# Kernel optimization log

Measured on AMD Instinct MI355X. Metric: run time of the kernel, lower is better.

## Reference

```python
import jax, jax.numpy as jnp
import numpy as np

M = 262144
GRID_SIZE = 1024
L1_BITS = 15            # 3 * log2(1024/32): top bits of morton give the 32^3 L1 cell
L1_CELLS = 32 * 32 * 32
MAX_EXT = 4             # 4^3 = 64 == oversized_threshold_voxels
OVERSIZED_THRESHOLD = 64
VOXEL_SIZE_FACTOR = 3.0
CLIP_Q = 0.01
PAD = 0.1
CHI2_95_3 = 7.814727903251179  # chi2.ppf(0.95, df=3)
SENTINEL = np.int64(1 << 30)   # larger than any 30-bit morton code
EPS = 1e-7


def quat_to_rotmat(q):
    q = q / (jnp.linalg.norm(q, axis=-1, keepdims=True) + EPS)
    w, x, y, z = q[..., 0], q[..., 1], q[..., 2], q[..., 3]
    R = jnp.stack([
        1 - 2 * (y * y + z * z), 2 * (x * y - w * z), 2 * (x * z + w * y),
        2 * (x * y + w * z), 1 - 2 * (x * x + z * z), 2 * (y * z - w * x),
        2 * (x * z - w * y), 2 * (y * z + w * x), 1 - 2 * (x * x + y * y),
    ], axis=-1)
    return R.reshape(q.shape[:-1] + (3, 3))


def expand_bits_10(v):
    x = v.astype(jnp.uint32)
    x = (x | (x << 16)) & jnp.uint32(0x030000FF)
    x = (x | (x << 8)) & jnp.uint32(0x0300F00F)
    x = (x | (x << 4)) & jnp.uint32(0x030C30C3)
    x = (x | (x << 2)) & jnp.uint32(0x09249249)
    return x


def encode_morton(c):
    # c: [..., 3] int32 grid coords -> uint32 morton
    ci = jnp.clip(c, 0, 1023).astype(jnp.uint32)
    return (expand_bits_10(ci[..., 0]) << 2) | (expand_bits_10(ci[..., 1]) << 1) | expand_bits_10(ci[..., 2])


def setup_inputs() -> dict:
    key = jax.random.key(0)
    k1, k2, k3 = jax.random.split(key, 3)
    positions = jax.random.normal(k1, (M, 3), dtype=jnp.float32) * 10.0
    scales = jax.random.uniform(k2, (M, 3), dtype=jnp.float32) * 0.02 + 0.002
    quats = jax.random.normal(k3, (M, 4), dtype=jnp.float32)
    return {"positions": positions, "scales": scales, "quats": quats}


def reference(positions, scales, quats):
    m = positions.shape[0]
    # 1) per-sphere AABB from confidence ellipsoid of Sigma = R diag(s^2) R^T
    R = quat_to_rotmat(quats)
    k = jnp.sqrt(jnp.float32(CHI2_95_3))
    radius = k * jnp.sqrt(jnp.einsum('mij,mj->mi', R * R, scales * scales) + 1e-12)  # [M,3]
    min_corners = positions - radius
    max_corners = positions + radius
    # robust global AABB: quantile clip + padding
    gmin = jnp.quantile(min_corners, CLIP_Q, axis=0)
    gmax = jnp.quantile(max_corners, 1.0 - CLIP_Q, axis=0)
    extent = gmax - gmin
    global_min = gmin - PAD * extent
    voxel_size = jnp.median(radius[:, 0]) * VOXEL_SIZE_FACTOR
    # 2) enumerate sphere-voxel pairs (fixed 4x4x4 window per sphere, masked)
    g_min = jnp.clip(jnp.floor((min_corners - global_min) / voxel_size).astype(jnp.int32), 0, GRID_SIZE - 1)
    g_max = jnp.clip(jnp.floor((max_corners - global_min) / voxel_size).astype(jnp.int32), 0, GRID_SIZE - 1)
    ext = g_max - g_min + 1                       # [M,3]
    nvox = ext[:, 0] * ext[:, 1] * ext[:, 2]
    oversized = (nvox > OVERSIZED_THRESHOLD) | jnp.any(ext > MAX_EXT, axis=-1)
    d = jnp.arange(MAX_EXT, dtype=jnp.int32)
    offs = jnp.stack(jnp.meshgrid(d, d, d, indexing='ij'), axis=-1).reshape(-1, 3)  # [64,3]
    coords = g_min[:, None, :] + offs[None, :, :]  # [M,64,3]
    valid = jnp.all(offs[None] < ext[:, None, :], axis=-1) & (~oversized[:, None])  # [M,64]
    morton = encode_morton(coords).astype(jnp.int64)  # [M,64]
    morton = jnp.where(valid, morton, SENTINEL)
    sphere_id = jnp.where(valid, jnp.arange(m, dtype=jnp.int32)[:, None], jnp.int32(-1))
    mf = morton.reshape(-1)
    sf = sphere_id.reshape(-1)
    # 3) sort pairs by morton code (invalid/sentinel entries compact to the end)
    order = jnp.argsort(mf)
    sm = mf[order]
    ss = sf[order]
    total_pairs = jnp.sum(valid).astype(jnp.int32)
    # 4) L1 lookup table: start offset of each 32^3 coarse cell in sorted pairs
    l1keys = sm >> L1_BITS
    cells = jnp.arange(L1_CELLS, dtype=sm.dtype)
    left = jnp.searchsorted(l1keys, cells, side='left')
    right = jnp.searchsorted(l1keys, cells, side='right')
    l1_offsets = jnp.where(right > left, left, -1).astype(jnp.int32)
    # unique occupied voxels
    valid_s = sm < SENTINEL
    is_new = jnp.concatenate([valid_s[:1], valid_s[1:] & (sm[1:] != sm[:-1])])
    num_unique = jnp.sum(is_new).astype(jnp.int32)
    # 5) precompute sphere data: Sigma^{-1} = R diag(s^-2) R^T, Gaussian norm factor
    inv_s2 = 1.0 / (scales * scales + 1e-12)
    cov_inv = jnp.einsum('mij,mj,mkj->mik', R, inv_s2, R)
    norm_factor = 1.0 / (((2.0 * jnp.pi) ** 1.5) * jnp.prod(scales, axis=-1) + EPS)
    return (sm, ss, oversized.astype(jnp.int32), l1_offsets, total_pairs, num_unique,
            global_min.astype(jnp.float32), voxel_size.astype(jnp.float32), cov_inv, norm_factor)
```

## Files before the change

### kernel.cpp

```cpp
#include <hip/hip_runtime.h>
#include <stdint.h>
#include <math.h>

#define MS 262144
#define NPAIR 16777216
#define RBINS 1024
#define SORT_TILE 2048
#define MAXC (4u*1048576u)
#define OUTK_BLOCKS 2048

#define OFF_SELHIST   0u
#define OFF_SELSTATE  114688u
#define OFF_SELVALS   114800u
#define OFF_DEVN      114856u
#define OFF_DEVU      114860u
#define OFF_SCANPART  114864u
#define OFF_SCANBASE  115888u
#define OFF_PARAMS    116912u
#define WS_ZERO_BYTES 131072u
#define OFF_CORNERS   ((size_t)131072)
#define OFF_GMP       (OFF_CORNERS + (size_t)7*MS*4)
#define OFF_EXTP      (OFF_GMP + (size_t)MS*4)
#define OFF_COUNTS    (OFF_EXTP + (size_t)MS*4)
#define OFF_OFFS      (OFF_COUNTS + (size_t)MS*4)
#define FIXED_WS      (OFF_OFFS + (size_t)MS*4)

#define O_SM   0u
#define O_SS   16777216u
#define O_OV   33554432u
#define O_L1   33816576u
#define O_TP   33849344u
#define O_NU   33849345u
#define O_GMIN 33849346u
#define O_VOX  33849349u
#define O_COV  33849350u
#define O_NF   36208646u

__constant__ uint32_t RANKS[14] = {2621u,2622u,2621u,2622u,2621u,2622u,
                                   259521u,259522u,259521u,259522u,259521u,259522u,
                                   131071u,131072u};

__device__ __forceinline__ uint32_t fkey(float f) {
  uint32_t u = __float_as_uint(f);
  return (u & 0x80000000u) ? ~u : (u | 0x80000000u);
}
__device__ __forceinline__ float unfkey(uint32_t u) {
  uint32_t b = (u & 0x80000000u) ? (u ^ 0x80000000u) : ~u;
  return __uint_as_float(b);
}
__device__ __forceinline__ uint32_t expand10(uint32_t x) {
  x = (x | (x << 16)) & 0x030000FFu;
  x = (x | (x << 8))  & 0x0300F00Fu;
  x = (x | (x << 4))  & 0x030C30C3u;
  x = (x | (x << 2))  & 0x09249249u;
  return x;
}

__global__ void sphere_kernel(const float* __restrict__ pos,
                              const float* __restrict__ scl,
                              const float* __restrict__ qt,
                              float* __restrict__ corners,
                              float* __restrict__ out) {
#pragma clang fp contract(off)
  int i = blockIdx.x * 256 + threadIdx.x;
  if (i >= MS) return;
  float qw = qt[4*i+0], qx = qt[4*i+1], qy = qt[4*i+2], qz = qt[4*i+3];
  float ssum = (((qw*qw) + (qx*qx)) + (qy*qy)) + (qz*qz);
  float nrm = sqrtf(ssum);
  float den = nrm + 1e-7f;
  float w = qw / den, x = qx / den, y = qy / den, z = qz / den;
  float xx=x*x, yy=y*y, zz=z*z, xy=x*y, xz=x*z, yz=y*z, wx=w*x, wy=w*y, wz=w*z;
  float R00 = 1.0f - 2.0f*(yy+zz);
  float R01 = 2.0f*(xy-wz);
  float R02 = 2.0f*(xz+wy);
  float R10 = 2.0f*(xy+wz);
  float R11 = 1.0f - 2.0f*(xx+zz);
  float R12 = 2.0f*(yz-wx);
  float R20 = 2.0f*(xz-wy);
  float R21 = 2.0f*(yz+wx);
  float R22 = 1.0f - 2.0f*(xx+yy);
  float s0 = scl[3*i+0], s1 = scl[3*i+1], s2c = scl[3*i+2];
  float t0 = s0*s0, t1 = s1*s1, t2 = s2c*s2c;
  const float KC = sqrtf(7.814727903251179f);
  float d0 = (((R00*R00)*t0) + ((R01*R01)*t1)) + ((R02*R02)*t2);
  float d1 = (((R10*R10)*t0) + ((R11*R11)*t1)) + ((R12*R12)*t2);
  float d2 = (((R20*R20)*t0) + ((R21*R21)*t1)) + ((R22*R22)*t2);
  float r0 = KC * sqrtf(d0 + 1e-12f);
  float r1 = KC * sqrtf(d1 + 1e-12f);
  float r2 = KC * sqrtf(d2 + 1e-12f);
  float px = pos[3*i+0], py = pos[3*i+1], pz = pos[3*i+2];
  corners[(size_t)0*MS+i] = px - r0;
  corners[(size_t)1*MS+i] = py - r1;
  corners[(size_t)2*MS+i] = pz - r2;
  corners[(size_t)3*MS+i] = px + r0;
  corners[(size_t)4*MS+i] = py + r1;
  corners[(size_t)5*MS+i] = pz + r2;
  corners[(size_t)6*MS+i] = r0;
  float i0 = 1.0f / (t0 + 1e-12f);
  float i1 = 1.0f / (t1 + 1e-12f);
  float i2 = 1.0f / (t2 + 1e-12f);
  float* cv = out + O_COV + (size_t)i*9;
  cv[0] = ((R00*i0)*R00 + (R01*i1)*R01) + (R02*i2)*R02;
  cv[1] = ((R00*i0)*R10 + (R01*i1)*R11) + (R02*i2)*R12;
  cv[2] = ((R00*i0)*R20 + (R01*i1)*R21) + (R02*i2)*R22;
  cv[3] = ((R10*i0)*R00 + (R11*i1)*R01) + (R12*i2)*R02;
  cv[4] = ((R10*i0)*R10 + (R11*i1)*R11) + (R12*i2)*R12;
  cv[5] = ((R10*i0)*R20 + (R11*i1)*R21) + (R12*i2)*R22;
  cv[6] = ((R20*i0)*R00 + (R21*i1)*R01) + (R22*i2)*R02;
  cv[7] = ((R20*i0)*R10 + (R21*i1)*R11) + (R22*i2)*R12;
  cv[8] = ((R20*i0)*R20 + (R21*i1)*R21) + (R22*i2)*R22;
  out[O_NF + i] = 1.0f / ((15.749609945722419f * ((s0*s1)*s2c)) + 1e-7f);
}

__global__ void sel_hist(const float* __restrict__ corners,
                         const uint32_t* __restrict__ selstate,
                         uint32_t* __restrict__ selhist, int round) {
  __shared__ uint32_t h[2048];
  int j = blockIdx.y;
  const float* a = corners + (size_t)(j >> 1) * MS;
  for (int d = threadIdx.x; d < 2048; d += 256) h[d] = 0;
  __syncthreads();
  uint32_t pref = 0;
  int dshift = 21, pshift = 31, maskb = 2047;
  if (round == 1) { pref = selstate[2*j]; dshift = 10; pshift = 21; }
  else if (round == 2) { pref = selstate[2*j]; dshift = 0; pshift = 10; maskb = 1023; }
  int base = blockIdx.x * 4096;
  for (int t = threadIdx.x; t < 4096; t += 256) {
    uint32_t u = fkey(a[base + t]);
    bool ok = (round == 0) || ((u >> pshift) == pref);
    if (ok) atomicAdd(&h[(u >> dshift) & (uint32_t)maskb], 1u);
  }
  __syncthreads();
  uint32_t* gh = selhist + (size_t)j * 2048;
  for (int d = threadIdx.x; d < 2048; d += 256) {
    uint32_t c = h[d];
    if (c) atomicAdd(&gh[d], c);
  }
}

__global__ void sel_fin(uint32_t* __restrict__ selhist,
                        uint32_t* __restrict__ selstate,
                        uint32_t* __restrict__ selvals, int round) {
  __shared__ uint32_t part[256];
  int j = blockIdx.x;
  uint32_t* h = selhist + (size_t)j * 2048;
  int bins = (round == 2) ? 1024 : 2048;
  uint32_t s = 0;
  int gbase = threadIdx.x * 8;
  #pragma unroll
  for (int b = 0; b < 8; b++) { int d = gbase + b; s += (d < bins) ? h[d] : 0u; }
  part[threadIdx.x] = s;
  __syncthreads();
  if (threadIdx.x == 0) {
    uint32_t rank = (round == 0) ? RANKS[j] : selstate[2*j+1];
    uint32_t run = 0; int grp = 0;
    for (; grp < 255; grp++) { uint32_t p = part[grp]; if (rank < run + p) break; run += p; }
    uint32_t dig = 0;
    for (int b = 0; b < 8; b++) {
      int d = grp*8 + b; uint32_t c = (d < bins) ? h[d] : 0u;
      if (rank < run + c) { dig = (uint32_t)d; break; }
      run += c;
    }
    rank -= run;
    uint32_t pref;
    if (round == 0) pref = dig;
    else if (round == 1) pref = (selstate[2*j] << 11) | dig;
    else pref = (selstate[2*j] << 10) | dig;
    selstate[2*j] = pref; selstate[2*j+1] = rank;
    if (round == 2) selvals[j] = pref;
  }
  __syncthreads();
  for (int d = threadIdx.x; d < 2048; d += 256) h[d] = 0;
}

__global__ void params_kernel(const uint32_t* __restrict__ selvals,
                              float* __restrict__ params, float* __restrict__ out) {
#pragma clang fp contract(off)
  if (threadIdx.x != 0 || blockIdx.x != 0) return;
  float v[14];
  for (int j = 0; j < 14; j++) v[j] = unfkey(selvals[j]);
  float g1   = (float)(0.01 * 262143.0 - 2621.0);
  float t2   = (float)(0.99 * 262143.0 - 259521.0);
  float omt2 = 1.0f - t2;
  float gmin[3], gmax[3];
  for (int a = 0; a < 3; a++) {
    float lo = v[2*a], hi = v[2*a+1];
    float d  = hi - lo;
    gmin[a] = lo + d * g1;
  }
  for (int a = 0; a < 3; a++) {
    float lo = v[6+2*a], hi = v[7+2*a];
    float d  = hi - lo;
    gmax[a] = hi - d * omt2;
  }
  float med = (v[12] + v[13]) * 0.5f;
  float vox = med * 3.0f;
  for (int a = 0; a < 3; a++) {
    float ext = gmax[a] - gmin[a];
    float gm  = gmin[a] - 0.1f * ext;
    params[a] = gm;
    out[O_GMIN + a] = gm;
  }
  params[3] = vox;
  out[O_VOX] = vox;
}

__global__ void grid_kernel(const float* __restrict__ corners,
                            const float* __restrict__ params,
                            uint32_t* __restrict__ gmp, uint32_t* __restrict__ extp,
                            uint32_t* __restrict__ counts, float* __restrict__ out) {
#pragma clang fp contract(off)
  int i = blockIdx.x * 256 + threadIdx.x;
  if (i >= MS) return;
  float vox = params[3];
  int g0[3], g1[3];
  for (int a = 0; a < 3; a++) {
    float gm = params[a];
    float lo = corners[(size_t)a*MS + i];
    float hi = corners[(size_t)(a+3)*MS + i];
    int lq = (int)floorf((lo - gm) / vox);
    int hq = (int)floorf((hi - gm) / vox);
    g0[a] = min(max(lq, 0), 1023);
    g1[a] = min(max(hq, 0), 1023);
  }
  int ex = g1[0]-g0[0]+1, ey = g1[1]-g0[1]+1, ez = g1[2]-g0[2]+1;
  int nv = ex*ey*ez;
  bool ovs = (nv > 64) || (ex > 4) || (ey > 4) || (ez > 4);
  out[O_OV + i] = ovs ? 1.0f : 0.0f;
  gmp[i] = (uint32_t)g0[0] | ((uint32_t)g0[1] << 10) | ((uint32_t)g0[2] << 20);
  extp[i] = ovs ? 0u : ((uint32_t)ex | ((uint32_t)ey << 8) | ((uint32_t)ez << 16));
  counts[i] = ovs ? 0u : (uint32_t)nv;
}

__global__ void scan1(const uint32_t* __restrict__ counts, uint32_t* __restrict__ offs,
                      uint32_t* __restrict__ part) {
  __shared__ uint32_t sh[256];
  int b = blockIdx.x, tid = threadIdx.x;
  int base = b * 1024 + tid * 4;
  uint32_t v0 = counts[base], v1 = counts[base+1], v2 = counts[base+2], v3 = counts[base+3];
  uint32_t sum = v0+v1+v2+v3;
  sh[tid] = sum; __syncthreads();
  for (int off = 1; off < 256; off <<= 1) {
    uint32_t x = (tid >= off) ? sh[tid-off] : 0u;
    __syncthreads();
    sh[tid] += x;
    __syncthreads();
  }
  uint32_t excl = sh[tid] - sum;
  if (tid == 255) part[b] = sh[255];
  offs[base] = excl; offs[base+1] = excl+v0; offs[base+2] = excl+v0+v1; offs[base+3] = excl+v0+v1+v2;
}

__global__ void scan2(const uint32_t* __restrict__ part, uint32_t* __restrict__ sbase,
                      uint32_t* __restrict__ devN, uint32_t cap) {
  __shared__ uint32_t sh[256];
  int tid = threadIdx.x;
  uint32_t v = part[tid];
  sh[tid] = v; __syncthreads();
  for (int off = 1; off < 256; off <<= 1) {
    uint32_t x = (tid >= off) ? sh[tid-off] : 0u;
    __syncthreads();
    sh[tid] += x;
    __syncthreads();
  }
  sbase[tid] = sh[tid] - v;
  if (tid == 255) *devN = min(sh[255], cap);
}

__global__ void emit_pairs(const uint32_t* __restrict__ gmp, const uint32_t* __restrict__ extp,
                           const uint32_t* __restrict__ offs, const uint32_t* __restrict__ sbase,
                           uint32_t* __restrict__ akey, uint32_t* __restrict__ aval,
                           uint32_t cap) {
  int i = blockIdx.x * 256 + threadIdx.x;
  if (i >= MS) return;
  uint32_t ep = extp[i];
  if (!ep) return;
  uint32_t p = offs[i] + sbase[i >> 10];
  if (p >= cap) return;
  uint32_t gp = gmp[i];
  int gx = gp & 1023, gy = (gp >> 10) & 1023, gz = (gp >> 20) & 1023;
  int ex = ep & 255, ey = (ep >> 8) & 255, ez = (ep >> 16) & 255;
  for (int dx = 0; dx < ex; dx++) {
    uint32_t mx = expand10((uint32_t)(gx+dx)) << 2;
    for (int dy = 0; dy < ey; dy++) {
      uint32_t mxy = mx | (expand10((uint32_t)(gy+dy)) << 1);
      for (int dz = 0; dz < ez; dz++) {
        if (p < cap) { akey[p] = mxy | expand10((uint32_t)(gz+dz)); aval[p] = (uint32_t)i; }
        p++;
      }
    }
  }
}

__global__ void rdx_hist(const uint32_t* __restrict__ keys, const uint32_t* __restrict__ devN,
                         uint32_t* __restrict__ ctab, int shift, int nt) {
  __shared__ uint32_t h[RBINS];
  int t = blockIdx.x;
  for (int i = threadIdx.x; i < RBINS; i += 256) h[i] = 0;
  __syncthreads();
  int N = (int)*devN;
  int base = t * SORT_TILE;
  int cnt = min(SORT_TILE, N - base);
  if (cnt == SORT_TILE) {
    const uint4* k4 = reinterpret_cast<const uint4*>(keys + base);
    #pragma unroll
    for (int j = 0; j < 2; j++) {
      uint4 k = k4[j * 256 + threadIdx.x];
      atomicAdd(&h[(k.x >> shift) & (RBINS-1)], 1u);
      atomicAdd(&h[(k.y >> shift) & (RBINS-1)], 1u);
      atomicAdd(&h[(k.z >> shift) & (RBINS-1)], 1u);
      atomicAdd(&h[(k.w >> shift) & (RBINS-1)], 1u);
    }
  } else {
    for (int i = threadIdx.x; i < cnt; i += 256)
      atomicAdd(&h[(keys[base + i] >> shift) & (RBINS - 1)], 1u);
  }
  __syncthreads();
  for (int i = threadIdx.x; i < RBINS; i += 256) ctab[(size_t)i * nt + t] = h[i];
}

__global__ void rdx_colscan(uint32_t* __restrict__ ctab, uint32_t* __restrict__ dtot, int nt) {
  __shared__ uint32_t sh[256];
  int d = blockIdx.x, tid = threadIdx.x;
  uint32_t* row = ctab + (size_t)d * nt;
  int per = nt >> 8;
  uint32_t v[8];
  uint32_t s = 0;
  const uint4* r4 = reinterpret_cast<const uint4*>(row + tid * per);
  #pragma unroll
  for (int j = 0; j < 2; j++) {
    uint4 q = r4[j];
    v[j*4+0]=q.x; v[j*4+1]=q.y; v[j*4+2]=q.z; v[j*4+3]=q.w;
    s += q.x+q.y+q.z+q.w;
  }
  sh[tid] = s; __syncthreads();
  for (int off = 1; off < 256; off <<= 1) {
    uint32_t x = (tid >= off) ? sh[tid - off] : 0u;
    __syncthreads();
    sh[tid] += x;
    __syncthreads();
  }
  uint32_t excl = sh[tid] - s;
  uint4* w4 = reinterpret_cast<uint4*>(row + tid * per);
  #pragma unroll
  for (int j = 0; j < 2; j++) {
    uint4 q;
    q.x = excl; excl += v[j*4+0];
    q.y = excl; excl += v[j*4+1];
    q.z = excl; excl += v[j*4+2];
    q.w = excl; excl += v[j*4+3];
    w4[j] = q;
  }
  if (tid == 255) dtot[d] = excl;
}

__global__ void rdx_basescan(const uint32_t* __restrict__ dtot, uint32_t* __restrict__ dbase) {
  __shared__ uint32_t sh[256];
  int tid = threadIdx.x;
  uint32_t run = 0;
  for (int c = 0; c < RBINS; c += 256) {
    uint32_t v = dtot[c + tid];
    sh[tid] = v; __syncthreads();
    for (int off = 1; off < 256; off <<= 1) {
      uint32_t x = (tid >= off) ? sh[tid - off] : 0u;
      __syncthreads();
      sh[tid] += x;
      __syncthreads();
    }
    dbase[c + tid] = run + (sh[tid] - v);
    uint32_t tot = sh[255];
    __syncthreads();
    run += tot;
  }
}

__global__ __launch_bounds__(256) void rdx_scatter(
    const uint32_t* __restrict__ keyIn, const uint32_t* __restrict__ valIn,
    uint32_t* __restrict__ keyOut, uint32_t* __restrict__ valOut,
    const uint32_t* __restrict__ ctab, const uint32_t* __restrict__ dbase,
    const uint32_t* __restrict__ devN, int shift, int nt) {
  __shared__ uint32_t cnt[4][RBINS];
  __shared__ uint32_t goff[RBINS];
  int tile = blockIdx.x;
  int N = (int)*devN;
  int base = tile * SORT_TILE;
  if (base >= N) return;
  int count = min(SORT_TILE, N - base);
  int w = threadIdx.x >> 6, lane = threadIdx.x & 63;
  for (int i = threadIdx.x; i < 4*RBINS; i += 256) (&cnt[0][0])[i] = 0;
  for (int i = threadIdx.x; i < RBINS; i += 256)
    goff[i] = dbase[i] + ctab[(size_t)i * nt + tile];
  __syncthreads();
  const int ITER = SORT_TILE / 256;
  uint32_t karr[ITER], varr[ITER], drk[ITER];
  uint64_t lmask = (lane == 0) ? 0ull : ((~0ull) >> (64 - lane));
  #pragma unroll
  for (int i = 0; i < ITER; i++) {
    int idx = w * (SORT_TILE/4) + (i << 6) + lane;
    bool act = idx < count;
    uint32_t key = 0, val = 0;
    if (act) { key = keyIn[base + idx]; val = valIn[base + idx]; }
    uint32_t dig = (key >> shift) & (RBINS - 1);
    uint64_t mask = __ballot(act);
    #pragma unroll
    for (int b = 0; b < 10; b++) {
      uint64_t bal = __ballot(act && ((dig >> b) & 1));
      mask &= ((dig >> b) & 1) ? bal : ~bal;
    }
    int ldr = (mask != 0ull) ? (__ffsll((unsigned long long)mask) - 1) : 0;
    int rig = __popcll(mask & lmask);
    int bcnt = __popcll(mask);
    uint32_t basec = 0;
    if (act && lane == ldr) { basec = cnt[w][dig]; cnt[w][dig] = basec + (uint32_t)bcnt; }
    basec = (uint32_t)__shfl((int)basec, ldr);
    drk[i] = dig | ((basec + (uint32_t)rig) << 16);
    karr[i] = key; varr[i] = val;
  }
  __syncthreads();
  for (int d = threadIdx.x; d < RBINS; d += 256) {
    uint32_t c0 = cnt[0][d], c1 = cnt[1][d], c2 = cnt[2][d];
    cnt[0][d] = 0; cnt[1][d] = c0; cnt[2][d] = c0 + c1; cnt[3][d] = c0 + c1 + c2;
  }
  __syncthreads();
  #pragma unroll
  for (int i = 0; i < ITER; i++) {
    int idx = w * (SORT_TILE/4) + (i << 6) + lane;
    if (idx < count) {
      uint32_t dig = drk[i] & (RBINS - 1);
      uint32_t r = drk[i] >> 16;
      uint32_t dst = goff[dig] + cnt[w][dig] + r;
      keyOut[dst] = karr[i]; valOut[dst] = varr[i];
    }
  }
}

__global__ void l1_search(const uint32_t* __restrict__ keys, const uint32_t* __restrict__ devN,
                          float* __restrict__ out) {
  int c = blockIdx.x * 256 + threadIdx.x;
  int N = (int)*devN;
  uint32_t target = (uint32_t)c << 15;
  int lo = 0, hi = N;
  while (lo < hi) { int mid = (lo + hi) >> 1; if (keys[mid] < target) lo = mid + 1; else hi = mid; }
  bool occ = (lo < N) && ((keys[lo] >> 15) == (uint32_t)c);
  out[O_L1 + c] = occ ? (float)lo : -1.0f;
}

__global__ void out_kernel(const uint32_t* __restrict__ bkey, const uint32_t* __restrict__ bval,
                           float* __restrict__ out, const uint32_t* __restrict__ devN,
                           uint32_t* __restrict__ devU) {
  int N = (int)*devN;
  uint32_t lcount = 0;
  const int nGroups = NPAIR / 4;
  const float4 smSent = make_float4(1073741824.0f, 1073741824.0f, 1073741824.0f, 1073741824.0f);
  const float4 ssSent = make_float4(-1.0f, -1.0f, -1.0f, -1.0f);
  for (int g = blockIdx.x * 256 + threadIdx.x; g < nGroups; g += OUTK_BLOCKS * 256) {
    int i = g << 2;
    float4 sm, ss;
    if (i + 3 < N) {
      uint4 k = *reinterpret_cast<const uint4*>(&bkey[i]);
      uint4 v = *reinterpret_cast<const uint4*>(&bval[i]);
      sm = make_float4((float)k.x, (float)k.y, (float)k.z, (float)k.w);
      ss = make_float4((float)(int)v.x, (float)(int)v.y, (float)(int)v.z, (float)(int)v.w);
      uint32_t kprev = (i > 0) ? bkey[i-1] : 0u;
      lcount += (uint32_t)((i == 0) || (k.x != kprev))
              + (uint32_t)(k.y != k.x) + (uint32_t)(k.z != k.y) + (uint32_t)(k.w != k.z);
    } else if (i >= N) {
      sm = smSent; ss = ssSent;
    } else {
      float smv[4], ssv[4];
      #pragma unroll
      for (int j = 0; j < 4; j++) {
        int idx = i + j;
        if (idx < N) {
          uint32_t k = bkey[idx];
          smv[j] = (float)k; ssv[j] = (float)(int)bval[idx];
          uint32_t kp = (idx > 0) ? bkey[idx-1] : 0u;
          lcount += (uint32_t)((idx == 0) || (k != kp));
        } else { smv[j] = 1073741824.0f; ssv[j] = -1.0f; }
      }
      sm = make_float4(smv[0], smv[1], smv[2], smv[3]);
      ss = make_float4(ssv[0], ssv[1], ssv[2], ssv[3]);
    }
    *reinterpret_cast<float4*>(&out[O_SM + (uint32_t)i]) = sm;
    *reinterpret_cast<float4*>(&out[O_SS + (uint32_t)i]) = ss;
  }
  #pragma unroll
  for (int o = 32; o > 0; o >>= 1) lcount += (uint32_t)__shfl_down((int)lcount, o);
  if ((threadIdx.x & 63) == 0 && lcount) atomicAdd(devU, lcount);
}

__global__ void scalars_kernel(const uint32_t* __restrict__ devN, const uint32_t* __restrict__ devU,
                               float* __restrict__ out) {
  if (threadIdx.x == 0 && blockIdx.x == 0) {
    out[O_TP] = (float)*devN;
    out[O_NU] = (float)*devU;
  }
}

extern "C" void kernel_launch(void* const* d_in, const int* in_sizes, int n_in,
                              void* d_out, int out_size, void* d_ws, size_t ws_size,
                              hipStream_t stream) {
  const float* pos = (const float*)d_in[0];
  const float* scl = (const float*)d_in[1];
  const float* qt  = (const float*)d_in[2];
  float* out = (float*)d_out;
  char* ws = (char*)d_ws;
  uint32_t* selhist  = (uint32_t*)(ws + OFF_SELHIST);
  uint32_t* selstate = (uint32_t*)(ws + OFF_SELSTATE);
  uint32_t* selvals  = (uint32_t*)(ws + OFF_SELVALS);
  uint32_t* devN     = (uint32_t*)(ws + OFF_DEVN);
  uint32_t* devU     = (uint32_t*)(ws + OFF_DEVU);
  uint32_t* scanPart = (uint32_t*)(ws + OFF_SCANPART);
  uint32_t* scanBase = (uint32_t*)(ws + OFF_SCANBASE);
  float*    params   = (float*)(ws + OFF_PARAMS);
  float*    corners  = (float*)(ws + OFF_CORNERS);
  uint32_t* gmp      = (uint32_t*)(ws + OFF_GMP);
  uint32_t* extp     = (uint32_t*)(ws + OFF_EXTP);
  uint32_t* counts   = (uint32_t*)(ws + OFF_COUNTS);
  uint32_t* offs     = (uint32_t*)(ws + OFF_OFFS);

  size_t avail = (ws_size > FIXED_WS + 16384) ? (ws_size - FIXED_WS - 16384) : 0;
  size_t cmax  = avail / 18;
  uint32_t C = (uint32_t)((cmax / 1048576) * 1048576);
  if (C < 1048576u) C = 1048576u;
  if (C > MAXC) C = MAXC;
  int NT = (int)(C / SORT_TILE);

  char* dyn = ws + FIXED_WS;
  uint32_t* ak    = (uint32_t*)(dyn);
  uint32_t* av    = (uint32_t*)(dyn + (size_t)4*C);
  uint32_t* bk2   = (uint32_t*)(dyn + (size_t)8*C);
  uint32_t* bv2   = (uint32_t*)(dyn + (size_t)12*C);
  uint32_t* ctab  = (uint32_t*)(dyn + (size_t)16*C);
  uint32_t* dtot  = (uint32_t*)(dyn + (size_t)18*C);
  uint32_t* dbase = (uint32_t*)(dyn + (size_t)18*C + 4096);

  hipMemsetAsync(d_ws, 0, WS_ZERO_BYTES, stream);
  sphere_kernel<<<MS/256, 256, 0, stream>>>(pos, scl, qt, corners, out);
  for (int r = 0; r < 3; r++) {
    sel_hist<<<dim3(64,14), 256, 0, stream>>>(corners, selstate, selhist, r);
    sel_fin<<<14, 256, 0, stream>>>(selhist, selstate, selvals, r);
  }
  params_kernel<<<1, 64, 0, stream>>>(selvals, params, out);
  grid_kernel<<<MS/256, 256, 0, stream>>>(corners, params, gmp, extp, counts, out);
  scan1<<<256, 256, 0, stream>>>(counts, offs, scanPart);
  scan2<<<1, 256, 0, stream>>>(scanPart, scanBase, devN, C);
  emit_pairs<<<MS/256, 256, 0, stream>>>(gmp, extp, offs, scanBase, ak, av, C);
  rdx_hist<<<NT, 256, 0, stream>>>(ak, devN, ctab, 0, NT);
  rdx_colscan<<<RBINS, 256, 0, stream>>>(ctab, dtot, NT);
  rdx_basescan<<<1, 256, 0, stream>>>(dtot, dbase);
  rdx_scatter<<<NT, 256, 0, stream>>>(ak, av, bk2, bv2, ctab, dbase, devN, 0, NT);
  rdx_hist<<<NT, 256, 0, stream>>>(bk2, devN, ctab, 10, NT);
  rdx_colscan<<<RBINS, 256, 0, stream>>>(ctab, dtot, NT);
  rdx_basescan<<<1, 256, 0, stream>>>(dtot, dbase);
  rdx_scatter<<<NT, 256, 0, stream>>>(bk2, bv2, ak, av, ctab, dbase, devN, 10, NT);
  rdx_hist<<<NT, 256, 0, stream>>>(ak, devN, ctab, 20, NT);
  rdx_colscan<<<RBINS, 256, 0, stream>>>(ctab, dtot, NT);
  rdx_basescan<<<1, 256, 0, stream>>>(dtot, dbase);
  rdx_scatter<<<NT, 256, 0, stream>>>(ak, av, bk2, bv2, ctab, dbase, devN, 20, NT);
  l1_search<<<128, 256, 0, stream>>>(bk2, devN, out);
  out_kernel<<<OUTK_BLOCKS, 256, 0, stream>>>(bk2, bv2, out, devN, devU);
  scalars_kernel<<<1, 64, 0, stream>>>(devN, devU, out);
}
```

Measured before the change: 477.6 us.

## Merge follow-up kernels via last-block tickets and enlarge radix sort tiles

Folds sel_fin into sel_pass, scan2 into scan1, rdx_basescan into rdx_colscan, and l1_search plus scalars_kernel into out_kernel. Each merge uses an atomic ticket so the last finishing block does the tail work, which removes about a dozen small kernel launches and their serialization gaps. Radix sort tiles grow from 2048 to 8192 keys and scatter uses 512 threads with 8 wave counters, giving fewer tiles and a smaller count table. The costs are fence and atomic overhead, a serial tail in the last block, and more LDS per scatter block, which may lower occupancy.

```diff
diff --git a/kernel.cpp b/kernel.cpp
--- a/kernel.cpp
+++ b/kernel.cpp
@@ -5,7 +5,7 @@
 #define MS 262144
 #define NPAIR 16777216
 #define RBINS 1024
-#define SORT_TILE 2048
+#define SORT_TILE 8192
 #define MAXC (4u*1048576u)
 #define OUTK_BLOCKS 2048
 
@@ -17,6 +17,7 @@
 #define OFF_SCANPART  114864u
 #define OFF_SCANBASE  115888u
 #define OFF_PARAMS    116912u
+#define OFF_TICKETS   117952u
 #define WS_ZERO_BYTES 131072u
 #define OFF_CORNERS   ((size_t)131072)
 #define OFF_GMP       (OFF_CORNERS + (size_t)7*MS*4)
@@ -24,6 +25,11 @@
 #define OFF_COUNTS    (OFF_EXTP + (size_t)MS*4)
 #define OFF_OFFS      (OFF_COUNTS + (size_t)MS*4)
 #define FIXED_WS      (OFF_OFFS + (size_t)MS*4)
+
+#define TK_SCAN1 0
+#define TK_COL   1
+#define TK_OUT   4
+#define TK_SEL   5
 
 #define O_SM   0u
 #define O_SS   16777216u
@@ -112,10 +118,14 @@
   out[O_NF + i] = 1.0f / ((15.749609945722419f * ((s0*s1)*s2c)) + 1e-7f);
 }
 
-__global__ void sel_hist(const float* __restrict__ corners,
-                         const uint32_t* __restrict__ selstate,
-                         uint32_t* __restrict__ selhist, int round) {
+__global__ void sel_pass(const float* __restrict__ corners,
+                         uint32_t* __restrict__ selstate,
+                         uint32_t* __restrict__ selhist,
+                         uint32_t* __restrict__ selvals,
+                         uint32_t* __restrict__ tickets, int round) {
   __shared__ uint32_t h[2048];
+  __shared__ uint32_t part[256];
+  __shared__ uint32_t lastFlag;
   int j = blockIdx.y;
   const float* a = corners + (size_t)(j >> 1) * MS;
   for (int d = threadIdx.x; d < 2048; d += 256) h[d] = 0;
@@ -136,19 +146,18 @@
     uint32_t c = h[d];
     if (c) atomicAdd(&gh[d], c);
   }
-}
-
-__global__ void sel_fin(uint32_t* __restrict__ selhist,
-                        uint32_t* __restrict__ selstate,
-                        uint32_t* __restrict__ selvals, int round) {
-  __shared__ uint32_t part[256];
-  int j = blockIdx.x;
-  uint32_t* h = selhist + (size_t)j * 2048;
+  __threadfence();
+  __syncthreads();
+  if (threadIdx.x == 0)
+    lastFlag = (atomicAdd(&tickets[TK_SEL + round*14 + j], 1u) == 63u) ? 1u : 0u;
+  __syncthreads();
+  if (!lastFlag) return;
+  __threadfence();
   int bins = (round == 2) ? 1024 : 2048;
   uint32_t s = 0;
   int gbase = threadIdx.x * 8;
   #pragma unroll
-  for (int b = 0; b < 8; b++) { int d = gbase + b; s += (d < bins) ? h[d] : 0u; }
+  for (int b = 0; b < 8; b++) { int d = gbase + b; s += (d < bins) ? gh[d] : 0u; }
   part[threadIdx.x] = s;
   __syncthreads();
   if (threadIdx.x == 0) {
@@ -157,20 +166,20 @@
     for (; grp < 255; grp++) { uint32_t p = part[grp]; if (rank < run + p) break; run += p; }
     uint32_t dig = 0;
     for (int b = 0; b < 8; b++) {
-      int d = grp*8 + b; uint32_t c = (d < bins) ? h[d] : 0u;
+      int d = grp*8 + b; uint32_t c = (d < bins) ? gh[d] : 0u;
       if (rank < run + c) { dig = (uint32_t)d; break; }
       run += c;
     }
     rank -= run;
-    uint32_t pref;
-    if (round == 0) pref = dig;
-    else if (round == 1) pref = (selstate[2*j] << 11) | dig;
-    else pref = (selstate[2*j] << 10) | dig;
-    selstate[2*j] = pref; selstate[2*j+1] = rank;
-    if (round == 2) selvals[j] = pref;
-  }
-  __syncthreads();
-  for (int d = threadIdx.x; d < 2048; d += 256) h[d] = 0;
+    uint32_t prefn;
+    if (round == 0) prefn = dig;
+    else if (round == 1) prefn = (selstate[2*j] << 11) | dig;
+    else prefn = (selstate[2*j] << 10) | dig;
+    selstate[2*j] = prefn; selstate[2*j+1] = rank;
+    if (round == 2) selvals[j] = prefn;
+  }
+  __syncthreads();
+  for (int d = threadIdx.x; d < 2048; d += 256) gh[d] = 0;
 }
 
 __global__ void params_kernel(const uint32_t* __restrict__ selvals,
@@ -233,8 +242,11 @@
 }
 
 __global__ void scan1(const uint32_t* __restrict__ counts, uint32_t* __restrict__ offs,
-                      uint32_t* __restrict__ part) {
+                      uint32_t* __restrict__ part, uint32_t* __restrict__ sbase,
+                      uint32_t* __restrict__ devN, uint32_t* __restrict__ tickets,
+                      uint32_t cap) {
   __shared__ uint32_t sh[256];
+  __shared__ uint32_t lastFlag;
   int b = blockIdx.x, tid = threadIdx.x;
   int base = b * 1024 + tid * 4;
   uint32_t v0 = counts[base], v1 = counts[base+1], v2 = counts[base+2], v3 = counts[base+3];
@@ -249,12 +261,12 @@
   uint32_t excl = sh[tid] - sum;
   if (tid == 255) part[b] = sh[255];
   offs[base] = excl; offs[base+1] = excl+v0; offs[base+2] = excl+v0+v1; offs[base+3] = excl+v0+v1+v2;
-}
-
-__global__ void scan2(const uint32_t* __restrict__ part, uint32_t* __restrict__ sbase,
-                      uint32_t* __restrict__ devN, uint32_t cap) {
-  __shared__ uint32_t sh[256];
-  int tid = threadIdx.x;
+  __threadfence();
+  __syncthreads();
+  if (tid == 0) lastFlag = (atomicAdd(&tickets[TK_SCAN1], 1u) == 255u) ? 1u : 0u;
+  __syncthreads();
+  if (!lastFlag) return;
+  __threadfence();
   uint32_t v = part[tid];
   sh[tid] = v; __syncthreads();
   for (int off = 1; off < 256; off <<= 1) {
@@ -304,7 +316,7 @@
   if (cnt == SORT_TILE) {
     const uint4* k4 = reinterpret_cast<const uint4*>(keys + base);
     #pragma unroll
-    for (int j = 0; j < 2; j++) {
+    for (int j = 0; j < SORT_TILE/1024; j++) {
       uint4 k = k4[j * 256 + threadIdx.x];
       atomicAdd(&h[(k.x >> shift) & (RBINS-1)], 1u);
       atomicAdd(&h[(k.y >> shift) & (RBINS-1)], 1u);
@@ -319,44 +331,35 @@
   for (int i = threadIdx.x; i < RBINS; i += 256) ctab[(size_t)i * nt + t] = h[i];
 }
 
-__global__ void rdx_colscan(uint32_t* __restrict__ ctab, uint32_t* __restrict__ dtot, int nt) {
+__global__ void rdx_colscan(uint32_t* __restrict__ ctab, uint32_t* __restrict__ dtot,
+                            uint32_t* __restrict__ dbase, uint32_t* __restrict__ tickets,
+                            int nt, int pass) {
+  __shared__ uint32_t lds[512];
   __shared__ uint32_t sh[256];
+  __shared__ uint32_t lastFlag;
   int d = blockIdx.x, tid = threadIdx.x;
   uint32_t* row = ctab + (size_t)d * nt;
-  int per = nt >> 8;
-  uint32_t v[8];
-  uint32_t s = 0;
-  const uint4* r4 = reinterpret_cast<const uint4*>(row + tid * per);
-  #pragma unroll
-  for (int j = 0; j < 2; j++) {
-    uint4 q = r4[j];
-    v[j*4+0]=q.x; v[j*4+1]=q.y; v[j*4+2]=q.z; v[j*4+3]=q.w;
-    s += q.x+q.y+q.z+q.w;
-  }
-  sh[tid] = s; __syncthreads();
-  for (int off = 1; off < 256; off <<= 1) {
-    uint32_t x = (tid >= off) ? sh[tid - off] : 0u;
-    __syncthreads();
-    sh[tid] += x;
-    __syncthreads();
-  }
-  uint32_t excl = sh[tid] - s;
-  uint4* w4 = reinterpret_cast<uint4*>(row + tid * per);
-  #pragma unroll
-  for (int j = 0; j < 2; j++) {
-    uint4 q;
-    q.x = excl; excl += v[j*4+0];
-    q.y = excl; excl += v[j*4+1];
-    q.z = excl; excl += v[j*4+2];
-    q.w = excl; excl += v[j*4+3];
-    w4[j] = q;
-  }
-  if (tid == 255) dtot[d] = excl;
-}
-
-__global__ void rdx_basescan(const uint32_t* __restrict__ dtot, uint32_t* __restrict__ dbase) {
-  __shared__ uint32_t sh[256];
-  int tid = threadIdx.x;
+  int s0 = tid, s1 = tid + 256;
+  uint32_t v0 = (s0 < nt) ? row[s0] : 0u;
+  uint32_t v1 = (s1 < nt) ? row[s1] : 0u;
+  lds[s0] = v0; lds[s1] = v1;
+  __syncthreads();
+  for (int off = 1; off < 512; off <<= 1) {
+    uint32_t a0 = (s0 >= off) ? lds[s0 - off] : 0u;
+    uint32_t a1 = (s1 >= off) ? lds[s1 - off] : 0u;
+    __syncthreads();
+    lds[s0] += a0; lds[s1] += a1;
+    __syncthreads();
+  }
+  if (s0 < nt) row[s0] = lds[s0] - v0;
+  if (s1 < nt) row[s1] = lds[s1] - v1;
+  if (tid == 255) dtot[d] = lds[511];
+  __threadfence();
+  __syncthreads();
+  if (tid == 0) lastFlag = (atomicAdd(&tickets[TK_COL + pass], 1u) == (uint32_t)(RBINS-1)) ? 1u : 0u;
+  __syncthreads();
+  if (!lastFlag) return;
+  __threadfence();
   uint32_t run = 0;
   for (int c = 0; c < RBINS; c += 256) {
     uint32_t v = dtot[c + tid];
@@ -374,12 +377,12 @@
   }
 }
 
-__global__ __launch_bounds__(256) void rdx_scatter(
+__global__ __launch_bounds__(512) void rdx_scatter(
     const uint32_t* __restrict__ keyIn, const uint32_t* __restrict__ valIn,
     uint32_t* __restrict__ keyOut, uint32_t* __restrict__ valOut,
     const uint32_t* __restrict__ ctab, const uint32_t* __restrict__ dbase,
     const uint32_t* __restrict__ devN, int shift, int nt) {
-  __shared__ uint32_t cnt[4][RBINS];
+  __shared__ uint32_t cnt[8][RBINS];
   __shared__ uint32_t goff[RBINS];
   int tile = blockIdx.x;
   int N = (int)*devN;
@@ -387,16 +390,16 @@
   if (base >= N) return;
   int count = min(SORT_TILE, N - base);
   int w = threadIdx.x >> 6, lane = threadIdx.x & 63;
-  for (int i = threadIdx.x; i < 4*RBINS; i += 256) (&cnt[0][0])[i] = 0;
-  for (int i = threadIdx.x; i < RBINS; i += 256)
+  for (int i = threadIdx.x; i < 8*RBINS; i += 512) (&cnt[0][0])[i] = 0;
+  for (int i = threadIdx.x; i < RBINS; i += 512)
     goff[i] = dbase[i] + ctab[(size_t)i * nt + tile];
   __syncthreads();
-  const int ITER = SORT_TILE / 256;
+  const int ITER = SORT_TILE / 512;
   uint32_t karr[ITER], varr[ITER], drk[ITER];
   uint64_t lmask = (lane == 0) ? 0ull : ((~0ull) >> (64 - lane));
   #pragma unroll
   for (int i = 0; i < ITER; i++) {
-    int idx = w * (SORT_TILE/4) + (i << 6) + lane;
+    int idx = w * (SORT_TILE/8) + (i << 6) + lane;
     bool act = idx < count;
     uint32_t key = 0, val = 0;
     if (act) { key = keyIn[base + idx]; val = valIn[base + idx]; }
@@ -417,14 +420,15 @@
     karr[i] = key; varr[i] = val;
   }
   __syncthreads();
-  for (int d = threadIdx.x; d < RBINS; d += 256) {
-    uint32_t c0 = cnt[0][d], c1 = cnt[1][d], c2 = cnt[2][d];
-    cnt[0][d] = 0; cnt[1][d] = c0; cnt[2][d] = c0 + c1; cnt[3][d] = c0 + c1 + c2;
+  for (int d = threadIdx.x; d < RBINS; d += 512) {
+    uint32_t run = 0;
+    #pragma unroll
+    for (int ww = 0; ww < 8; ww++) { uint32_t c = cnt[ww][d]; cnt[ww][d] = run; run += c; }
   }
   __syncthreads();
   #pragma unroll
   for (int i = 0; i < ITER; i++) {
-    int idx = w * (SORT_TILE/4) + (i << 6) + lane;
+    int idx = w * (SORT_TILE/8) + (i << 6) + lane;
     if (idx < count) {
       uint32_t dig = drk[i] & (RBINS - 1);
       uint32_t r = drk[i] >> 16;
@@ -434,26 +438,24 @@
   }
 }
 
-__global__ void l1_search(const uint32_t* __restrict__ keys, const uint32_t* __restrict__ devN,
-                          float* __restrict__ out) {
-  int c = blockIdx.x * 256 + threadIdx.x;
-  int N = (int)*devN;
-  uint32_t target = (uint32_t)c << 15;
-  int lo = 0, hi = N;
-  while (lo < hi) { int mid = (lo + hi) >> 1; if (keys[mid] < target) lo = mid + 1; else hi = mid; }
-  bool occ = (lo < N) && ((keys[lo] >> 15) == (uint32_t)c);
-  out[O_L1 + c] = occ ? (float)lo : -1.0f;
-}
-
 __global__ void out_kernel(const uint32_t* __restrict__ bkey, const uint32_t* __restrict__ bval,
                            float* __restrict__ out, const uint32_t* __restrict__ devN,
-                           uint32_t* __restrict__ devU) {
+                           uint32_t* __restrict__ devU, uint32_t* __restrict__ tickets) {
+  __shared__ uint32_t lastFlag;
   int N = (int)*devN;
+  int gtid = blockIdx.x * 256 + threadIdx.x;
+  if (gtid < 32768) {
+    uint32_t target = (uint32_t)gtid << 15;
+    int lo = 0, hi = N;
+    while (lo < hi) { int mid = (lo + hi) >> 1; if (bkey[mid] < target) lo = mid + 1; else hi = mid; }
+    bool occ = (lo < N) && ((bkey[lo] >> 15) == (uint32_t)gtid);
+    out[O_L1 + gtid] = occ ? (float)lo : -1.0f;
+  }
   uint32_t lcount = 0;
   const int nGroups = NPAIR / 4;
   const float4 smSent = make_float4(1073741824.0f, 1073741824.0f, 1073741824.0f, 1073741824.0f);
   const float4 ssSent = make_float4(-1.0f, -1.0f, -1.0f, -1.0f);
-  for (int g = blockIdx.x * 256 + threadIdx.x; g < nGroups; g += OUTK_BLOCKS * 256) {
+  for (int g = gtid; g < nGroups; g += OUTK_BLOCKS * 256) {
     int i = g << 2;
     float4 sm, ss;
     if (i + 3 < N) {
@@ -487,12 +489,14 @@
   #pragma unroll
   for (int o = 32; o > 0; o >>= 1) lcount += (uint32_t)__shfl_down((int)lcount, o);
   if ((threadIdx.x & 63) == 0 && lcount) atomicAdd(devU, lcount);
-}
-
-__global__ void scalars_kernel(const uint32_t* __restrict__ devN, const uint32_t* __restrict__ devU,
-                               float* __restrict__ out) {
-  if (threadIdx.x == 0 && blockIdx.x == 0) {
-    out[O_TP] = (float)*devN;
+  __threadfence();
+  __syncthreads();
+  if (threadIdx.x == 0)
+    lastFlag = (atomicAdd(&tickets[TK_OUT], 1u) == (uint32_t)(OUTK_BLOCKS-1)) ? 1u : 0u;
+  __syncthreads();
+  if (lastFlag && threadIdx.x == 0) {
+    __threadfence();
+    out[O_TP] = (float)N;
     out[O_NU] = (float)*devU;
   }
 }
@@ -513,6 +517,7 @@
   uint32_t* scanPart = (uint32_t*)(ws + OFF_SCANPART);
   uint32_t* scanBase = (uint32_t*)(ws + OFF_SCANBASE);
   float*    params   = (float*)(ws + OFF_PARAMS);
+  uint32_t* tickets  = (uint32_t*)(ws + OFF_TICKETS);
   float*    corners  = (float*)(ws + OFF_CORNERS);
   uint32_t* gmp      = (uint32_t*)(ws + OFF_GMP);
   uint32_t* extp     = (uint32_t*)(ws + OFF_EXTP);
@@ -520,7 +525,7 @@
   uint32_t* offs     = (uint32_t*)(ws + OFF_OFFS);
 
   size_t avail = (ws_size > FIXED_WS + 16384) ? (ws_size - FIXED_WS - 16384) : 0;
-  size_t cmax  = avail / 18;
+  size_t cmax  = avail / 17;
   uint32_t C = (uint32_t)((cmax / 1048576) * 1048576);
   if (C < 1048576u) C = 1048576u;
   if (C > MAXC) C = MAXC;
@@ -532,33 +537,25 @@
   uint32_t* bk2   = (uint32_t*)(dyn + (size_t)8*C);
   uint32_t* bv2   = (uint32_t*)(dyn + (size_t)12*C);
   uint32_t* ctab  = (uint32_t*)(dyn + (size_t)16*C);
-  uint32_t* dtot  = (uint32_t*)(dyn + (size_t)18*C);
-  uint32_t* dbase = (uint32_t*)(dyn + (size_t)18*C + 4096);
+  uint32_t* dtot  = (uint32_t*)(dyn + (size_t)16*C + (size_t)C/2);
+  uint32_t* dbase = (uint32_t*)(dyn + (size_t)16*C + (size_t)C/2 + 4096);
 
   hipMemsetAsync(d_ws, 0, WS_ZERO_BYTES, stream);
   sphere_kernel<<<MS/256, 256, 0, stream>>>(pos, scl, qt, corners, out);
-  for (int r = 0; r < 3; r++) {
-    sel_hist<<<dim3(64,14), 256, 0, stream>>>(corners, selstate, selhist, r);
-    sel_fin<<<14, 256, 0, stream>>>(selhist, selstate, selvals, r);
-  }
+  for (int r = 0; r < 3; r++)
+    sel_pass<<<dim3(64,14), 256, 0, stream>>>(corners, selstate, selhist, selvals, tickets, r);
   params_kernel<<<1, 64, 0, stream>>>(selvals, params, out);
   grid_kernel<<<MS/256, 256, 0, stream>>>(corners, params, gmp, extp, counts, out);
-  scan1<<<256, 256, 0, stream>>>(counts, offs, scanPart);
-  scan2<<<1, 256, 0, stream>>>(scanPart, scanBase, devN, C);
+  scan1<<<256, 256, 0, stream>>>(counts, offs, scanPart, scanBase, devN, tickets, C);
   emit_pairs<<<MS/256, 256, 0, stream>>>(gmp, extp, offs, scanBase, ak, av, C);
   rdx_hist<<<NT, 256, 0, stream>>>(ak, devN, ctab, 0, NT);
-  rdx_colscan<<<RBINS, 256, 0, stream>>>(ctab, dtot, NT);
-  rdx_basescan<<<1, 256, 0, stream>>>(dtot, dbase);
-  rdx_scatter<<<NT, 256, 0, stream>>>(ak, av, bk2, bv2, ctab, dbase, devN, 0, NT);
+  rdx_colscan<<<RBINS, 256, 0, stream>>>(ctab, dtot, dbase, tickets, NT, 0);
+  rdx_scatter<<<NT, 512, 0, stream>>>(ak, av, bk2, bv2, ctab, dbase, devN, 0, NT);
   rdx_hist<<<NT, 256, 0, stream>>>(bk2, devN, ctab, 10, NT);
-  rdx_colscan<<<RBINS, 256, 0, stream>>>(ctab, dtot, NT);
-  rdx_basescan<<<1, 256, 0, stream>>>(dtot, dbase);
-  rdx_scatter<<<NT, 256, 0, stream>>>(bk2, bv2, ak, av, ctab, dbase, devN, 10, NT);
+  rdx_colscan<<<RBINS, 256, 0, stream>>>(ctab, dtot, dbase, tickets, NT, 1);
+  rdx_scatter<<<NT, 512, 0, stream>>>(bk2, bv2, ak, av, ctab, dbase, devN, 10, NT);
   rdx_hist<<<NT, 256, 0, stream>>>(ak, devN, ctab, 20, NT);
-  rdx_colscan<<<RBINS, 256, 0, stream>>>(ctab, dtot, NT);
-  rdx_basescan<<<1, 256, 0, stream>>>(dtot, dbase);
-  rdx_scatter<<<NT, 256, 0, stream>>>(ak, av, bk2, bv2, ctab, dbase, devN, 20, NT);
-  l1_search<<<128, 256, 0, stream>>>(bk2, devN, out);
-  out_kernel<<<OUTK_BLOCKS, 256, 0, stream>>>(bk2, bv2, out, devN, devU);
-  scalars_kernel<<<1, 64, 0, stream>>>(devN, devU, out);
-}
+  rdx_colscan<<<RBINS, 256, 0, stream>>>(ctab, dtot, dbase, tickets, NT, 2);
+  rdx_scatter<<<NT, 512, 0, stream>>>(ak, av, bk2, bv2, ctab, dbase, devN, 20, NT);
+  out_kernel<<<OUTK_BLOCKS, 256, 0, stream>>>(bk2, bv2, out, devN, devU, tickets);
+}
```

Result: slower. 1.046 ms (+119.0%).
